# Kernel tuning notes

Hardware: AMD Instinct MI355X
Metric: run time of the kernel (lower is better)

Reference implementation:

```python
import jax, jax.numpy as jnp
import numpy as np


def setup_inputs() -> dict:
    key = jax.random.key(0)
    k1, k2, k3, k4, k5 = jax.random.split(key, 5)
    B, S, E, H = 1024, 512, 50, 50
    bound = 1.0 / np.sqrt(H)  # PyTorch LSTM init range
    hidden_state = jax.random.normal(k1, (B, S, E), dtype=jnp.float32)
    W_ih = jax.random.uniform(k2, (4 * H, E), dtype=jnp.float32, minval=-bound, maxval=bound)
    W_hh = jax.random.uniform(k3, (4 * H, H), dtype=jnp.float32, minval=-bound, maxval=bound)
    b_ih = jax.random.uniform(k4, (4 * H,), dtype=jnp.float32, minval=-bound, maxval=bound)
    b_hh = jax.random.uniform(k5, (4 * H,), dtype=jnp.float32, minval=-bound, maxval=bound)
    return {"hidden_state": hidden_state, "W_ih": W_ih, "W_hh": W_hh, "b_ih": b_ih, "b_hh": b_hh}


def reference(hidden_state, W_ih, W_hh, b_ih, b_hh):
    # hidden_state: (B, S, E). Single-layer unidirectional LSTM, h0=c0=0.
    B, S, E = hidden_state.shape
    H = W_hh.shape[1]
    # Precompute input-to-gate projections for all timesteps: (S, B, 4H)
    xg = jnp.einsum('bse,ge->sbg', hidden_state, W_ih) + (b_ih + b_hh)

    def step(carry, xt):
        h, c = carry
        gates = xt + h @ W_hh.T  # (B, 4H)
        i, f, g, o = jnp.split(gates, 4, axis=-1)  # PyTorch gate order i,f,g,o
        i = jax.nn.sigmoid(i)
        f = jax.nn.sigmoid(f)
        g = jnp.tanh(g)
        o = jax.nn.sigmoid(o)
        c = f * c + i * g
        h = o * jnp.tanh(c)
        return (h, c), None

    h0 = jnp.zeros((B, H), dtype=hidden_state.dtype)
    c0 = jnp.zeros((B, H), dtype=hidden_state.dtype)
    (h_final, _), _ = jax.lax.scan(step, (h0, c0), xg)
    # PyTorch returns h_n of shape (num_layers, B, H); module transposes to (B, num_layers, H)
    return h_final[:, None, :]
```

## Files before the change

### kernel.cpp

```cpp
#include <hip/hip_runtime.h>


typedef __attribute__((ext_vector_type(8))) _Float16 f16x8;
typedef __attribute__((ext_vector_type(4))) float f32x4;

__device__ __forceinline__ float fast_sigmoid(float z) {
  return __builtin_amdgcn_rcpf(1.0f + __expf(-z));
}
__device__ __forceinline__ float fast_tanh(float z) {
  return 1.0f - 2.0f * __builtin_amdgcn_rcpf(1.0f + __expf(2.0f * z));
}

__global__ __launch_bounds__(512, 1) void lstm_fused(
    const float* __restrict__ xg,
    const float* __restrict__ W_ih,
    const float* __restrict__ W_hh,
    const float* __restrict__ b_ih,
    const float* __restrict__ b_hh,
    float* __restrict__ out)
{
  constexpr int S = 512, E = 50, H = 50;
  const int tid  = threadIdx.x;
  const int lane = tid & 63;
  const int wv   = tid >> 6;
  const int c0   = blockIdx.x << 2;

  __shared__ __align__(16) unsigned char lds[6400];
  for (int i = tid; i < 6400 / 4; i += 512) reinterpret_cast<unsigned*>(lds)[i] = 0u;

  const int m  = lane & 15;
  const int kg = lane >> 4;
  const int tstart = 2 * wv;
  const int ntiles = (wv < 6) ? 2 : ((wv == 6) ? 1 : 0);

  f16x8 wfr[2][4];
  f32x4 bias[2];
#pragma unroll
  for (int i = 0; i < 2; ++i) {
    const int  mt    = tstart + i;
    const bool tv    = (i < ntiles);
    const int  j     = mt * 16 + m;
    const int  hh    = j >> 2, g = j & 3;
    const bool rowok = tv && (hh < H);
#pragma unroll
    for (int kt = 0; kt < 4; ++kt) {
      f16x8 s;
#pragma unroll
      for (int jj = 0; jj < 8; ++jj) {
        const int k = kt * 32 + kg * 8 + jj;
        float w = 0.0f;
        if (rowok) {
          if (k < 50)                  w = W_ih[(g * 50 + hh) * 50 + k];
          else if (k >= 64 && k < 114) w = W_hh[(g * 50 + hh) * 50 + (k - 64)];
        }
        s[jj] = (_Float16)w;
      }
      wfr[i][kt] = s;
    }
    f32x4 bv;
#pragma unroll
    for (int r = 0; r < 4; ++r) {
      const int jr = mt * 16 + kg * 4 + r;
      const int hr = jr >> 2, gr = jr & 3;
      bv[r] = (tv && hr < H) ? (b_ih[gr * 50 + hr] + b_hh[gr * 50 + hr]) : 0.0f;
    }
    bias[i] = bv;
  }

  const bool iscell = (tid < 200);
  const int  cchain = tid & 3;
  const int  ch     = tid >> 2;
  float cst = 0.0f;

  const bool isstg = (wv == 7);
  bool     sok[4];
  long     gb[4];
  unsigned la[4];
  float    A[4], B[4];
#pragma unroll
  for (int u = 0; u < 4; ++u) {
    const int xs = lane + 64 * u;
    sok[u] = isstg && (xs < 200);
    const int chn = sok[u] ? (xs / 50) : 0;
    const int e   = sok[u] ? (xs - 50 * chn) : 0;
    gb[u] = ((long)(c0 + chn) * S) * E + e;
    la[u] = (unsigned)(((e >> 5) << 8) + (chn << 6) + ((e & 31) << 1));
    A[u] = 0.f; B[u] = 0.f;
  }

  __syncthreads();

#pragma unroll
  for (int u = 0; u < 4; ++u) {
    if (sok[u]) {
      *reinterpret_cast<_Float16*>(lds + 0 * 512 + la[u]) = (_Float16)xg[gb[u] + 0 * E];
      *reinterpret_cast<_Float16*>(lds + 1 * 512 + la[u]) = (_Float16)xg[gb[u] + 1 * E];
    }
  }
#pragma unroll
  for (int u = 0; u < 4; ++u) {
    if (sok[u]) { A[u] = xg[gb[u] + 2 * E]; B[u] = xg[gb[u] + 3 * E]; }
  }
  __syncthreads();

  const int      bc  = lane & 3;
  const unsigned bro = (unsigned)((bc << 6) + (kg << 4));

  f32x4 xcur[2];
  {
    const f16x8 b0 = *reinterpret_cast<const f16x8*>(lds + 0u + bro);
    const f16x8 b1 = *reinterpret_cast<const f16x8*>(lds + 256u + bro);
#pragma unroll
    for (int i = 0; i < 2; ++i) {
      f32x4 a = bias[i];
      a = __builtin_amdgcn_mfma_f32_16x16x32_f16(wfr[i][0], b0, a, 0, 0, 0);
      a = __builtin_amdgcn_mfma_f32_16x16x32_f16(wfr[i][1], b1, a, 0, 0, 0);
      xcur[i] = a;
    }
  }

  auto phase1 = [&](int t, float (&P)[4]) {
    if (ntiles > 0) {
      const unsigned hs = 2048u + (unsigned)(t & 1) * 512u;
      const unsigned xs = (unsigned)((t + 1) & 3) * 512u;
      const f16x8 b2  = *reinterpret_cast<const f16x8*>(lds + hs + bro);
      const f16x8 b3  = *reinterpret_cast<const f16x8*>(lds + hs + 256u + bro);
      const f16x8 nb0 = *reinterpret_cast<const f16x8*>(lds + xs + bro);
      const f16x8 nb1 = *reinterpret_cast<const f16x8*>(lds + xs + 256u + bro);
#pragma unroll
      for (int i = 0; i < 2; ++i) {
        f32x4 a = xcur[i];
        a = __builtin_amdgcn_mfma_f32_16x16x32_f16(wfr[i][2], b2, a, 0, 0, 0);
        a = __builtin_amdgcn_mfma_f32_16x16x32_f16(wfr[i][3], b3, a, 0, 0, 0);
        if ((m < 4) && (i < ntiles)) {
          const int h = (tstart + i) * 4 + kg;
          *reinterpret_cast<f32x4*>(lds + 3072u + (unsigned)(h * 64 + m * 16)) = a;
        }
        f32x4 c = bias[i];
        c = __builtin_amdgcn_mfma_f32_16x16x32_f16(wfr[i][0], nb0, c, 0, 0, 0);
        c = __builtin_amdgcn_mfma_f32_16x16x32_f16(wfr[i][1], nb1, c, 0, 0, 0);
        xcur[i] = c;
      }
    } else if (isstg) {
      if (t + 2 < S) {
        const unsigned sl = (unsigned)((t + 2) & 3) * 512u;
#pragma unroll
        for (int u = 0; u < 4; ++u)
          if (sok[u]) *reinterpret_cast<_Float16*>(lds + sl + la[u]) = (_Float16)P[u];
        if (t + 4 < S) {
#pragma unroll
          for (int u = 0; u < 4; ++u)
            if (sok[u]) P[u] = xg[gb[u] + (long)(t + 4) * E];
        }
      }
    }
  };

  auto phase2 = [&](int t) {
    if (iscell) {
      const f32x4 g4 = *reinterpret_cast<const f32x4*>(lds + 3072u + (unsigned)(tid * 16));
      const float ig = fast_sigmoid(g4[0]);
      const float fg = fast_sigmoid(g4[1]);
      const float gg = fast_tanh   (g4[2]);
      const float og = fast_sigmoid(g4[3]);
      const float c  = fg * cst + ig * gg;
      cst = c;
      const float hv = og * fast_tanh(c);
      if (t == S - 1) {
        out[(long)(c0 + cchain) * H + ch] = hv;
      } else {
        *reinterpret_cast<_Float16*>(
            lds + 2048u + (unsigned)((t + 1) & 1) * 512u +
            (unsigned)(((ch >> 5) << 8) + (cchain << 6) + ((ch & 31) << 1))) = (_Float16)hv;
      }
    }
  };

  for (int t = 0; t < S; t += 2) {
    phase1(t, A);
    __syncthreads();
    phase2(t);
    __syncthreads();
    phase1(t + 1, B);
    __syncthreads();
    phase2(t + 1);
    __syncthreads();
  }
}

extern "C" void kernel_launch(void* const* d_in, const int* in_sizes, int n_in,
                              void* d_out, int out_size, void* d_ws, size_t ws_size,
                              hipStream_t stream) {
  const float* x    = (const float*)d_in[0];
  const float* W_ih = (const float*)d_in[1];
  const float* W_hh = (const float*)d_in[2];
  const float* b_ih = (const float*)d_in[3];
  const float* b_hh = (const float*)d_in[4];
  float* out = (float*)d_out;
  hipLaunchKernelGGL(lstm_fused, dim3(256), dim3(512), 0, stream,
                     x, W_ih, W_hh, b_ih, b_hh, out);
}
```

Before: 224.9 us.

## Fuse gate activation into MFMA waves via bpermute, halving barriers per step

Previously each timestep wrote gate pre-activations to LDS, synchronised, then had a separate set of threads read them for the cell update and synchronised again. Now each MFMA wave redistributes its accumulator values with ds_bpermute so its own lanes compute the LSTM cell update directly, leaving one barrier per timestep and dropping the gate staging buffer from LDS. This shortens the serial critical path of the recurrence. In exchange the MFMA waves do extra cross-lane permutes and the activation work is spread over fewer active lanes per wave.

Result: no change. 220.6 us (-1.9%).

```diff
diff --git a/kernel.cpp b/kernel.cpp
--- a/kernel.cpp
+++ b/kernel.cpp
@@ -25,8 +25,8 @@
   const int wv   = tid >> 6;
   const int c0   = blockIdx.x << 2;
 
-  __shared__ __align__(16) unsigned char lds[6400];
-  for (int i = tid; i < 6400 / 4; i += 512) reinterpret_cast<unsigned*>(lds)[i] = 0u;
+  __shared__ __align__(16) unsigned char lds[3072];
+  for (int i = tid; i < 3072 / 4; i += 512) reinterpret_cast<unsigned*>(lds)[i] = 0u;
 
   const int m  = lane & 15;
   const int kg = lane >> 4;
@@ -67,9 +67,13 @@
     bias[i] = bv;
   }
 
-  const bool iscell = (tid < 200);
-  const int  cchain = tid & 3;
-  const int  ch     = tid >> 2;
+  const int  al_i  = lane >> 4;
+  const int  al_kg = (lane >> 2) & 3;
+  const int  al_c  = lane & 3;
+  const int  al_h  = 4 * (tstart + al_i) + al_kg;
+  const bool al_ok = (lane < 16 * ntiles) && (al_h < H);
+  const int  bpaddr = ((((lane >> 2) & 3) * 16 + (lane & 3)) << 2);
+  const unsigned hwr = (unsigned)(((al_h >> 5) << 8) + (al_c << 6) + ((al_h & 31) << 1));
   float cst = 0.0f;
 
   const bool isstg = (wv == 7);
@@ -119,7 +123,7 @@
     }
   }
 
-  auto phase1 = [&](int t, float (&P)[4]) {
+  auto step = [&](int t, float (&P)[4]) {
     if (ntiles > 0) {
       const unsigned hs = 2048u + (unsigned)(t & 1) * 512u;
       const unsigned xs = (unsigned)((t + 1) & 3) * 512u;
@@ -127,19 +131,47 @@
       const f16x8 b3  = *reinterpret_cast<const f16x8*>(lds + hs + 256u + bro);
       const f16x8 nb0 = *reinterpret_cast<const f16x8*>(lds + xs + bro);
       const f16x8 nb1 = *reinterpret_cast<const f16x8*>(lds + xs + 256u + bro);
-#pragma unroll
-      for (int i = 0; i < 2; ++i) {
-        f32x4 a = xcur[i];
-        a = __builtin_amdgcn_mfma_f32_16x16x32_f16(wfr[i][2], b2, a, 0, 0, 0);
-        a = __builtin_amdgcn_mfma_f32_16x16x32_f16(wfr[i][3], b3, a, 0, 0, 0);
-        if ((m < 4) && (i < ntiles)) {
-          const int h = (tstart + i) * 4 + kg;
-          *reinterpret_cast<f32x4*>(lds + 3072u + (unsigned)(h * 64 + m * 16)) = a;
+
+      f32x4 acc0 = xcur[0];
+      acc0 = __builtin_amdgcn_mfma_f32_16x16x32_f16(wfr[0][2], b2, acc0, 0, 0, 0);
+      acc0 = __builtin_amdgcn_mfma_f32_16x16x32_f16(wfr[0][3], b3, acc0, 0, 0, 0);
+      f32x4 acc1 = xcur[1];
+      acc1 = __builtin_amdgcn_mfma_f32_16x16x32_f16(wfr[1][2], b2, acc1, 0, 0, 0);
+      acc1 = __builtin_amdgcn_mfma_f32_16x16x32_f16(wfr[1][3], b3, acc1, 0, 0, 0);
+
+      {
+        f32x4 c0v = bias[0];
+        c0v = __builtin_amdgcn_mfma_f32_16x16x32_f16(wfr[0][0], nb0, c0v, 0, 0, 0);
+        c0v = __builtin_amdgcn_mfma_f32_16x16x32_f16(wfr[0][1], nb1, c0v, 0, 0, 0);
+        xcur[0] = c0v;
+        f32x4 c1v = bias[1];
+        c1v = __builtin_amdgcn_mfma_f32_16x16x32_f16(wfr[1][0], nb0, c1v, 0, 0, 0);
+        c1v = __builtin_amdgcn_mfma_f32_16x16x32_f16(wfr[1][1], nb1, c1v, 0, 0, 0);
+        xcur[1] = c1v;
+      }
+
+      float gv[4];
+#pragma unroll
+      for (int r = 0; r < 4; ++r) {
+        const int p0 = __builtin_amdgcn_ds_bpermute(bpaddr, __float_as_int(acc0[r]));
+        const int p1 = __builtin_amdgcn_ds_bpermute(bpaddr, __float_as_int(acc1[r]));
+        gv[r] = __int_as_float((lane < 16) ? p0 : p1);
+      }
+
+      if (al_ok) {
+        const float ig = fast_sigmoid(gv[0]);
+        const float fg = fast_sigmoid(gv[1]);
+        const float gg = fast_tanh   (gv[2]);
+        const float og = fast_sigmoid(gv[3]);
+        const float c  = fg * cst + ig * gg;
+        cst = c;
+        const float hv = og * fast_tanh(c);
+        if (t == S - 1) {
+          out[(long)(c0 + al_c) * H + al_h] = hv;
+        } else {
+          *reinterpret_cast<_Float16*>(
+              lds + 2048u + (unsigned)((t + 1) & 1) * 512u + hwr) = (_Float16)hv;
         }
-        f32x4 c = bias[i];
-        c = __builtin_amdgcn_mfma_f32_16x16x32_f16(wfr[i][0], nb0, c, 0, 0, 0);
-        c = __builtin_amdgcn_mfma_f32_16x16x32_f16(wfr[i][1], nb1, c, 0, 0, 0);
-        xcur[i] = c;
       }
     } else if (isstg) {
       if (t + 2 < S) {
@@ -154,37 +186,12 @@
         }
       }
     }
+    __syncthreads();
   };
 
-  auto phase2 = [&](int t) {
-    if (iscell) {
-      const f32x4 g4 = *reinterpret_cast<const f32x4*>(lds + 3072u + (unsigned)(tid * 16));
-      const float ig = fast_sigmoid(g4[0]);
-      const float fg = fast_sigmoid(g4[1]);
-      const float gg = fast_tanh   (g4[2]);
-      const float og = fast_sigmoid(g4[3]);
-      const float c  = fg * cst + ig * gg;
-      cst = c;
-      const float hv = og * fast_tanh(c);
-      if (t == S - 1) {
-        out[(long)(c0 + cchain) * H + ch] = hv;
-      } else {
-        *reinterpret_cast<_Float16*>(
-            lds + 2048u + (unsigned)((t + 1) & 1) * 512u +
-            (unsigned)(((ch >> 5) << 8) + (cchain << 6) + ((ch & 31) << 1))) = (_Float16)hv;
-      }
-    }
-  };
-
   for (int t = 0; t < S; t += 2) {
-    phase1(t, A);
-    __syncthreads();
-    phase2(t);
-    __syncthreads();
-    phase1(t + 1, B);
-    __syncthreads();
-    phase2(t + 1);
-    __syncthreads();
+    step(t, A);
+    step(t + 1, B);
   }
 }
 
```
